# Kernel tuning notes

Measured on AMD Instinct MI355X. Metric: run time of the kernel, lower is better.

The kernel has to match this reference:

```python
import jax, jax.numpy as jnp
import numpy as np
import math

S, B, D_MODEL = 1024, 2, 1024
N_HEADS = 16
D_HEAD = D_MODEL // N_HEADS
C = 32  # compressed_len


def _xavier(key, shape):
    fan_in, fan_out = shape[-1], shape[-2] if len(shape) > 1 else shape[-1]
    limit = math.sqrt(6.0 / (fan_in + fan_out))
    return jax.random.uniform(key, shape, jnp.float32, -limit, limit)


def setup_inputs() -> dict:
    key = jax.random.key(0)
    ks = jax.random.split(key, 10)
    return {
        "x": jax.random.normal(ks[0], (S, B, D_MODEL), jnp.float32),
        "q_down": _xavier(ks[1], (C, D_MODEL)),
        "Wq": _xavier(ks[2], (D_MODEL, D_MODEL)),
        "bq": jnp.zeros((D_MODEL,), jnp.float32),
        "Wk": _xavier(ks[3], (D_MODEL, D_MODEL)),
        "bk": jnp.zeros((D_MODEL,), jnp.float32),
        "Wv": _xavier(ks[4], (D_MODEL, D_MODEL)),
        "bv": jnp.zeros((D_MODEL,), jnp.float32),
        "Wo": _xavier(ks[5], (D_MODEL, D_MODEL)),
        "bo": jnp.zeros((D_MODEL,), jnp.float32),
    }


def reference(x, q_down, Wq, bq, Wk, bk, Wv, bv, Wo, bo):
    # x: (s, b, d_model); causal=True, rope=None, dropout inactive (eval)
    s, b, d_model = x.shape
    h, dh = N_HEADS, D_HEAD
    scale = 1.0 / math.sqrt(dh)

    q_u = x @ Wq.T + bq                       # (s,b,dm)
    k_d = x @ Wk.T + bk
    v_d = x @ Wv.T + bv
    v_d_k = v_d @ Wk.T + bk
    v_d_v = v_d @ Wv.T + bv

    def heads(t):  # (s,b,dm) -> (b,h,s,dh)
        return t.reshape(s, b, h, dh).transpose(1, 2, 0, 3)

    q_u = heads(q_u) * scale
    k_d = heads(k_d)
    v_d_kv = jnp.concatenate([heads(v_d_k), heads(v_d_v)], axis=-1)  # (b,h,s,2dh)

    q_d = q_down.reshape(C, h, dh).transpose(1, 0, 2) * scale        # (h,c,dh)

    down = jnp.einsum('hcd,bhsd->bhcs', q_d, k_d)                    # (b,h,c,s)
    w = jnp.exp(down - jnp.max(down, axis=-1, keepdims=True))
    norm = jnp.cumsum(w, axis=-1)

    # (b,h,c,s,2dh): running compressed KV state
    kv_u = jnp.cumsum(w[..., None] * v_d_kv[:, :, None, :, :], axis=3) / norm[..., None]
    k_u, v_u = jnp.split(kv_u, 2, axis=-1)                           # each (b,h,c,s,dh)

    up = jnp.einsum('bhsd,bhcsd->bhsc', q_u, k_u)
    up = jax.nn.softmax(up, axis=-1)
    out = jnp.einsum('bhsc,bhcsd->bhsd', up, v_u)                    # (b,h,s,dh)

    out = out.transpose(2, 0, 1, 3).reshape(s, b, d_model)
    return out @ Wo.T + bo
```

## Files before the change

### kernel.cpp

```cpp
#include <hip/hip_runtime.h>
#include <cstdint>
#include <cstddef>

#define S_LEN 1024
#define BATCH 2
#define DM    1024
#define NH    16
#define DH    64
#define CC    32
#define SB    2048
#define TSD   128
#define NCHD  8

using short8 = __attribute__((ext_vector_type(8))) short;
using f32x4  = __attribute__((ext_vector_type(4))) float;

__device__ __forceinline__ float b2f(unsigned short u) {
    union { unsigned int i; float f; } v; v.i = ((unsigned int)u) << 16; return v.f;
}
__device__ __forceinline__ unsigned short f2b(float f) {
    union { float f; unsigned int i; } v; v.f = f;
    unsigned int x = v.i;
    unsigned int r = x + 0x7FFFu + ((x >> 16) & 1u);
    return (unsigned short)(r >> 16);
}

__device__ __forceinline__ void async_ld16(const unsigned short* g, unsigned short* l) {
    __builtin_amdgcn_global_load_lds(
        (const __attribute__((address_space(1))) unsigned int*)g,
        (__attribute__((address_space(3))) unsigned int*)l,
        16, 0, 0);
}

__global__ __launch_bounds__(256) void k_convert(
    const void* x, const void* qd,
    const void* wq, const void* wk, const void* wv, const void* wo,
    const void* bq, const void* bk, const void* bv, const void* bo,
    int* __restrict__ flag,
    unsigned short* xb, unsigned short* qdb,
    unsigned short* Wqb, unsigned short* Wkb, unsigned short* Wvb, unsigned short* Wob,
    float* biasf)
{
    __shared__ int cnt;
    if (threadIdx.x == 0) cnt = 0;
    __syncthreads();
    {
        const unsigned short* xs = (const unsigned short*)x;
        int local = 0;
        for (int i = threadIdx.x; i < 1024; i += 256) {
            unsigned e = (xs[i * 2] >> 7) & 0xFF;
            if (e >= 90 && e <= 160) local++;
        }
        atomicAdd(&cnt, local);
    }
    __syncthreads();
    const int isbf = (cnt >= 640);
    if (blockIdx.x == 0 && threadIdx.x == 0) *flag = isbf;

    const size_t tid = (size_t)blockIdx.x * 256 + threadIdx.x;
    const size_t stride = (size_t)gridDim.x * 256;

    auto cv = [&](const void* src, unsigned short* dst, size_t n) {
        if (isbf) {
            const short8* s = (const short8*)src;
            short8* d = (short8*)dst;
            for (size_t i = tid; i < n / 8; i += stride) d[i] = s[i];
        } else {
            const float4* s = (const float4*)src;
            for (size_t i = tid; i < n / 4; i += stride) {
                float4 v = s[i];
                ushort4 o;
                o.x = f2b(v.x); o.y = f2b(v.y); o.z = f2b(v.z); o.w = f2b(v.w);
                ((ushort4*)dst)[i] = o;
            }
        }
    };
    cv(x,  xb,  (size_t)SB * DM);
    cv(qd, qdb, (size_t)CC * DM);
    cv(wq, Wqb, (size_t)DM * DM);
    cv(wk, Wkb, (size_t)DM * DM);
    cv(wv, Wvb, (size_t)DM * DM);
    cv(wo, Wob, (size_t)DM * DM);
    for (size_t i = tid; i < 5 * DM; i += stride) {
        int w = (int)(i >> 10), o = (int)(i & 1023);
        float val;
        if (w == 4) val = 0.f;
        else {
            const void* bp = (w == 0) ? bq : ((w == 1) ? bk : ((w == 2) ? bv : bo));
            val = isbf ? b2f(((const unsigned short*)bp)[o]) : ((const float*)bp)[o];
        }
        biasf[i] = val;
    }
}

__global__ __launch_bounds__(256) void k_prep(const unsigned short* __restrict__ Wvb,
                                              const unsigned short* __restrict__ Wkb,
                                              const float* __restrict__ biasf,
                                              unsigned short* __restrict__ WvT,
                                              float* __restrict__ b2k,
                                              float* __restrict__ b2v)
{
    const int t = threadIdx.x;
    if (blockIdx.x < 128) {
        const int r0 = (blockIdx.x & 7) * 128;
        const int c0 = (blockIdx.x >> 3) * 64;
        __shared__ unsigned short T[128 * 68];
        for (int u = t; u < 128 * 8; u += 256) {
            int r = u >> 3, cb = (u & 7) * 8;
            *(short8*)&T[r * 68 + cb] = *(const short8*)&Wvb[(size_t)(r0 + r) * DM + c0 + cb];
        }
        __syncthreads();
        for (int u = t; u < 64 * 16; u += 256) {
            int c = u >> 4, r8 = (u & 15) * 8;
            short8 o;
#pragma unroll
            for (int k = 0; k < 8; ++k) o[k] = T[(r8 + k) * 68 + c];
            *(short8*)&WvT[(size_t)(c0 + c) * DM + r0 + r8] = o;
        }
    } else {
        const int idx = blockIdx.x - 128;
        const int set = idx >> 5;
        const int bx = idx & 31;
        const unsigned short* W = set ? Wvb : Wkb;
        const float* bvf = biasf + 2048;
        const float* badd = set ? (biasf + 2048) : (biasf + 1024);
        float* out = set ? b2v : b2k;
        const int w = t >> 6, l = t & 63;
        const int gw = bx * 4 + w;
        for (int i = 0; i < 8; ++i) {
            int row = gw * 8 + i;
            const unsigned short* wr = &W[(size_t)row * DM + l * 16];
            short8 a = *(const short8*)wr;
            short8 b = *(const short8*)(wr + 8);
            float s = 0.f;
#pragma unroll
            for (int j = 0; j < 8; ++j) {
                s += b2f((unsigned short)a[j]) * bvf[l * 16 + j];
                s += b2f((unsigned short)b[j]) * bvf[l * 16 + 8 + j];
            }
#pragma unroll
            for (int m = 1; m < 64; m <<= 1) s += __shfl_xor(s, m);
            if (l == 0) out[row] = s + badd[row];
        }
    }
}

struct GArg {
    const unsigned short* A;
    const unsigned short* Bt;
    const float* bias;
    void* out;
    float scale;
    int mode;
};

__device__ __forceinline__ int out_is_f32(int mode, const int* flag) {
    if (mode == 0) return 1;
    if (mode == 1) return 0;
    return (*flag == 0);
}

__global__ __launch_bounds__(256) void gemm_bt(GArg g0, GArg g1, GArg g2, GArg g3,
                                               const int* __restrict__ flag,
                                               int M, int N, int K)
{
    GArg ga = (blockIdx.z == 0) ? g0 : (blockIdx.z == 1) ? g1 : (blockIdx.z == 2) ? g2 : g3;
    const int m0 = blockIdx.y * 128;
    const int n0 = blockIdx.x * 128;
    __shared__ __align__(16) unsigned short As[2][128 * 32];
    __shared__ __align__(16) unsigned short Bs[2][128 * 32];
    const int t = threadIdx.x;
    const int w = t >> 6, l = t & 63;
    const int wy = w >> 1, wx = w & 1;
    const int lr = l >> 2;
    const int lk = (l & 3) * 8;
    const int ln = l & 15;
    const int lq = l >> 4;

    f32x4 acc[4][4] = {};

    const unsigned short* Ab0 = ga.A  + (size_t)(m0 + w * 32 +      lr) * K + lk;
    const unsigned short* Ab1 = ga.A  + (size_t)(m0 + w * 32 + 16 + lr) * K + lk;
    const unsigned short* Bb0 = ga.Bt + (size_t)(n0 + w * 32 +      lr) * K + lk;
    const unsigned short* Bb1 = ga.Bt + (size_t)(n0 + w * 32 + 16 + lr) * K + lk;

    for (int kk = 0; kk < K; kk += 64) {
#pragma unroll
        for (int hh = 0; hh < 2; ++hh) {
            async_ld16(Ab0 + kk + hh * 32, &As[hh][w * 1024]);
            async_ld16(Ab1 + kk + hh * 32, &As[hh][w * 1024 + 512]);
            async_ld16(Bb0 + kk + hh * 32, &Bs[hh][w * 1024]);
            async_ld16(Bb1 + kk + hh * 32, &Bs[hh][w * 1024 + 512]);
        }
        __syncthreads();
#pragma unroll
        for (int hh = 0; hh < 2; ++hh) {
            short8 af[4], bfr[4];
#pragma unroll
            for (int i = 0; i < 4; ++i)
                af[i] = *(const short8*)&As[hh][(wy * 64 + i * 16 + ln) * 32 + lq * 8];
#pragma unroll
            for (int j = 0; j < 4; ++j)
                bfr[j] = *(const short8*)&Bs[hh][(wx * 64 + j * 16 + ln) * 32 + lq * 8];
#pragma unroll
            for (int i = 0; i < 4; ++i)
#pragma unroll
                for (int j = 0; j < 4; ++j)
                    acc[i][j] = __builtin_amdgcn_mfma_f32_16x16x32_bf16(af[i], bfr[j], acc[i][j], 0, 0, 0);
        }
        __syncthreads();
    }

    const int f32o = out_is_f32(ga.mode, flag);
    const float sc = ga.scale;
#pragma unroll
    for (int j = 0; j < 4; ++j) {
        int col = n0 + wx * 64 + j * 16 + ln;
        float bv = ga.bias[col];
#pragma unroll
        for (int i = 0; i < 4; ++i) {
            int row0 = m0 + wy * 64 + i * 16 + lq * 4;
#pragma unroll
            for (int r = 0; r < 4; ++r) {
                float v = (acc[i][j][r] + bv) * sc;
                size_t idx = (size_t)(row0 + r) * N + col;
                if (f32o) ((float*)ga.out)[idx] = v;
                else      ((unsigned short*)ga.out)[idx] = f2b(v);
            }
        }
    }
}

__global__ __launch_bounds__(256) void gemm_bt_n64(GArg g0, GArg g1,
                                                   const int* __restrict__ flag,
                                                   int M, int N, int K)
{
    GArg ga = (blockIdx.z == 0) ? g0 : g1;
    const int m0 = blockIdx.y * 128;
    const int n0 = blockIdx.x * 64;
    __shared__ __align__(16) unsigned short As[2][128 * 32];
    __shared__ __align__(16) unsigned short Bs[2][64 * 32];
    const int t = threadIdx.x;
    const int w = t >> 6, l = t & 63;
    const int wy = w >> 1, wx = w & 1;
    const int lr = l >> 2;
    const int lk = (l & 3) * 8;
    const int ln = l & 15;
    const int lq = l >> 4;

    f32x4 acc[4][2] = {};

    const unsigned short* Ab0 = ga.A  + (size_t)(m0 + w * 32 +      lr) * K + lk;
    const unsigned short* Ab1 = ga.A  + (size_t)(m0 + w * 32 + 16 + lr) * K + lk;
    const unsigned short* Bb  = ga.Bt + (size_t)(n0 + w * 16 + lr) * K + lk;

    for (int kk = 0; kk < K; kk += 64) {
#pragma unroll
        for (int hh = 0; hh < 2; ++hh) {
            async_ld16(Ab0 + kk + hh * 32, &As[hh][w * 1024]);
            async_ld16(Ab1 + kk + hh * 32, &As[hh][w * 1024 + 512]);
            async_ld16(Bb  + kk + hh * 32, &Bs[hh][w * 512]);
        }
        __syncthreads();
#pragma unroll
        for (int hh = 0; hh < 2; ++hh) {
            short8 af[4], bfr[2];
#pragma unroll
            for (int i = 0; i < 4; ++i)
                af[i] = *(const short8*)&As[hh][(wy * 64 + i * 16 + ln) * 32 + lq * 8];
#pragma unroll
            for (int j = 0; j < 2; ++j)
                bfr[j] = *(const short8*)&Bs[hh][(wx * 32 + j * 16 + ln) * 32 + lq * 8];
#pragma unroll
            for (int i = 0; i < 4; ++i)
#pragma unroll
                for (int j = 0; j < 2; ++j)
                    acc[i][j] = __builtin_amdgcn_mfma_f32_16x16x32_bf16(af[i], bfr[j], acc[i][j], 0, 0, 0);
        }
        __syncthreads();
    }

    const int f32o = out_is_f32(ga.mode, flag);
    const float sc = ga.scale;
#pragma unroll
    for (int j = 0; j < 2; ++j) {
        int col = n0 + wx * 32 + j * 16 + ln;
        float bv = ga.bias[col];
#pragma unroll
        for (int i = 0; i < 4; ++i) {
            int row0 = m0 + wy * 64 + i * 16 + lq * 4;
#pragma unroll
            for (int r = 0; r < 4; ++r) {
                float v = (acc[i][j][r] + bv) * sc;
                size_t idx = (size_t)(row0 + r) * N + col;
                if (f32o) ((float*)ga.out)[idx] = v;
                else      ((unsigned short*)ga.out)[idx] = f2b(v);
            }
        }
    }
}

__global__ __launch_bounds__(256) void k_down(const unsigned short* __restrict__ kd,
                                              const unsigned short* __restrict__ qdw,
                                              float* __restrict__ wbuf,
                                              float* __restrict__ cmax,
                                              float* __restrict__ csum)
{
    const int bh = blockIdx.x;
    const int b = bh >> 4, h = bh & 15;
    const int chunk = blockIdx.y;
    const int s0 = chunk * TSD;
    const int t = threadIdx.x;

    __shared__ float qd[CC * DH];
    __shared__ float kt[TSD * DH];
    __shared__ float pm[CC * 8];
    __shared__ float cmf[CC];

    for (int idx = t; idx < CC * DH; idx += 256)
        qd[idx] = b2f(qdw[(idx >> 6) * DM + h * DH + (idx & 63)]);
    for (int u = t; u < TSD * DH / 8; u += 256) {
        int sl = u >> 3, d8 = (u & 7) * 8;
        short8 v = *(const short8*)&kd[(size_t)((s0 + sl) * BATCH + b) * DM + h * DH + d8];
#pragma unroll
        for (int j = 0; j < 8; ++j) kt[sl * DH + d8 + j] = b2f((unsigned short)v[j]);
    }
    __syncthreads();

    const int c = t & 31;
    float s16[16];
    float lmax = -3.4e38f;
    int it = 0;
    for (int idx = t; idx < CC * TSD; idx += 256, ++it) {
        int sl = idx >> 5;
        float s = 0.f;
#pragma unroll
        for (int d = 0; d < DH; d += 4) {
            float4 qa = *(const float4*)&qd[c * DH + d];
            float4 kb = *(const float4*)&kt[sl * DH + d];
            s += qa.x * kb.x + qa.y * kb.y + qa.z * kb.z + qa.w * kb.w;
        }
        s *= 0.125f;
        wbuf[((size_t)bh * CC + c) * S_LEN + s0 + sl] = s;
        s16[it] = s;
        lmax = fmaxf(lmax, s);
    }
    pm[c * 8 + (t >> 5)] = lmax;
    __syncthreads();
    if (t < CC) {
        float m = pm[t * 8];
#pragma unroll
        for (int g = 1; g < 8; ++g) m = fmaxf(m, pm[t * 8 + g]);
        cmf[t] = m;
        cmax[((size_t)bh * CC + t) * NCHD + chunk] = m;
    }
    __syncthreads();
    const float cm = cmf[c];
    float es = 0.f;
#pragma unroll
    for (int k = 0; k < 16; ++k) es += __expf(s16[k] - cm);
    pm[c * 8 + (t >> 5)] = es;
    __syncthreads();
    if (t < CC) {
        float ssum = pm[t * 8];
#pragma unroll
        for (int g = 1; g < 8; ++g) ssum += pm[t * 8 + g];
        csum[((size_t)bh * CC + t) * NCHD + chunk] = ssum;
    }
}

__global__ __launch_bounds__(256) void k_wapply(const float* __restrict__ wbuf,
                                                const float* __restrict__ cmax,
                                                const float* __restrict__ csum,
                                                unsigned short* __restrict__ wb,
                                                unsigned short* __restrict__ wT,
                                                float* __restrict__ invn)
{
    const int bh = blockIdx.x, seg = blockIdx.y;
    const int t = threadIdx.x;
    __shared__ float gm[CC];
    __shared__ float basep[CC];
    __shared__ float psum[CC][9];
    __shared__ unsigned short wTt[128 * 40];
    __shared__ float invt[128 * 36];

    if (t < CC) {
        const size_t cb = (size_t)(bh * CC + t) * NCHD;
        float m = cmax[cb];
#pragma unroll
        for (int g = 1; g < NCHD; ++g) m = fmaxf(m, cmax[cb + g]);
        gm[t] = m;
        float bsum = 0.f;
        for (int k = 0; k < seg; ++k)
            bsum += csum[cb + k] * __expf(cmax[cb + k] - m);
        basep[t] = bsum;
    }
    __syncthreads();

    const int c = t >> 3, sub = t & 7;
    const float gmc = gm[c];
    const size_t rbase = (size_t)bh * 32768 + c * 1024 + seg * 128 + sub * 16;
    float w16[16];
    float s = 0.f;
#pragma unroll
    for (int i = 0; i < 16; ++i) {
        float v = __expf(wbuf[rbase + i] - gmc);
        w16[i] = v; s += v;
    }
    psum[c][sub] = s;
    short8 o0, o1;
#pragma unroll
    for (int i = 0; i < 8; ++i) { o0[i] = f2b(w16[i]); o1[i] = f2b(w16[8 + i]); }
    *(short8*)&wb[rbase] = o0;
    *(short8*)&wb[rbase + 8] = o1;
#pragma unroll
    for (int i = 0; i < 16; ++i) wTt[(sub * 16 + i) * 40 + c] = f2b(w16[i]);
    __syncthreads();

    float run = basep[c];
    for (int k = 0; k < sub; ++k) run += psum[c][k];
#pragma unroll
    for (int i = 0; i < 16; ++i) {
        run += w16[i];
        invt[(sub * 16 + i) * 36 + c] = 1.0f / fmaxf(run, 1e-30f);
    }
    __syncthreads();

    for (int u = t; u < 128 * 4; u += 256) {
        int r = u >> 2, cb = (u & 3) * 8;
        *(short8*)&wT[(size_t)bh * 32768 + (seg * 128 + r) * 32 + cb] =
            *(const short8*)&wTt[r * 40 + cb];
    }
    for (int u = t; u < 128 * 8; u += 256) {
        int r = u >> 3, cb = (u & 7) * 4;
        *(float4*)&invn[(size_t)bh * 32768 + (seg * 128 + r) * 32 + cb] =
            *(const float4*)&invt[r * 36 + cb];
    }
}

__global__ __launch_bounds__(256) void k_state(const unsigned short* __restrict__ wb,
                                               const unsigned short* __restrict__ vdk,
                                               const unsigned short* __restrict__ vdv,
                                               float* __restrict__ Mst,
                                               float* __restrict__ NTst)
{
    const int bh = blockIdx.x, ch = blockIdx.y;
    const int b = bh >> 4, h = bh & 15;
    const int s0 = ch * 64;
    const int t = threadIdx.x;
    const int w = t >> 6, l = t & 63;
    const int ln = l & 15, lq = l >> 4;
    __shared__ __align__(16) unsigned short Ws[32 * 72];
    __shared__ __align__(16) unsigned short T1[64 * 72];
    __shared__ __align__(16) unsigned short T2[64 * 72];
    __shared__ __align__(16) unsigned short KT[64 * 72];
    __shared__ __align__(16) unsigned short VT[64 * 72];

    for (int u = t; u < 32 * 8; u += 256) {
        int r = u >> 3, cb = (u & 7) * 8;
        *(short8*)&Ws[r * 72 + cb] = *(const short8*)&wb[(size_t)bh * 32768 + r * 1024 + s0 + cb];
    }
    for (int u = t; u < 64 * 8; u += 256) {
        int r = u >> 3, cb = (u & 7) * 8;
        *(short8*)&T1[r * 72 + cb] =
            *(const short8*)&vdk[(size_t)((s0 + r) * BATCH + b) * DM + h * DH + cb];
        *(short8*)&T2[r * 72 + cb] =
            *(const short8*)&vdv[(size_t)((s0 + r) * BATCH + b) * DM + h * DH + cb];
    }
    __syncthreads();
    for (int u = t; u < 64 * 8; u += 256) {
        int d = u >> 3, s8 = (u & 7) * 8;
        short8 o1, o2;
#pragma unroll
        for (int k = 0; k < 8; ++k) {
            o1[k] = T1[(s8 + k) * 72 + d];
            o2[k] = T2[(s8 + k) * 72 + d];
        }
        *(short8*)&KT[d * 72 + s8] = o1;
        *(short8*)&VT[d * 72 + s8] = o2;
    }
    __syncthreads();

    f32x4 accM[2] = {};
#pragma unroll
    for (int ks = 0; ks < 2; ++ks) {
        short8 b8 = *(const short8*)&KT[(w * 16 + ln) * 72 + ks * 32 + lq * 8];
#pragma unroll
        for (int i = 0; i < 2; ++i) {
            short8 a8 = *(const short8*)&Ws[(i * 16 + ln) * 72 + ks * 32 + lq * 8];
            accM[i] = __builtin_amdgcn_mfma_f32_16x16x32_bf16(a8, b8, accM[i], 0, 0, 0);
        }
    }
#pragma unroll
    for (int i = 0; i < 2; ++i)
#pragma unroll
        for (int r = 0; r < 4; ++r)
            Mst[((size_t)(bh * 16 + ch) * 32 + i * 16 + lq * 4 + r) * 64 + w * 16 + ln] = accM[i][r];

    f32x4 accN[2] = {};
#pragma unroll
    for (int ks = 0; ks < 2; ++ks) {
        short8 a8 = *(const short8*)&VT[(w * 16 + ln) * 72 + ks * 32 + lq * 8];
#pragma unroll
        for (int j = 0; j < 2; ++j) {
            short8 b8 = *(const short8*)&Ws[(j * 16 + ln) * 72 + ks * 32 + lq * 8];
            accN[j] = __builtin_amdgcn_mfma_f32_16x16x32_bf16(a8, b8, accN[j], 0, 0, 0);
        }
    }
#pragma unroll
    for (int j = 0; j < 2; ++j)
#pragma unroll
        for (int r = 0; r < 4; ++r)
            NTst[((size_t)(bh * 16 + ch) * 64 + w * 16 + lq * 4 + r) * 32 + j * 16 + ln] = accN[j][r];
}

__global__ __launch_bounds__(256) void k_prefix(const float* __restrict__ Mst,
                                                const float* __restrict__ NTst,
                                                unsigned short* __restrict__ Mcum,
                                                unsigned short* __restrict__ NTcum)
{
    const int bh = blockIdx.x;
    const float* src = blockIdx.y ? NTst : Mst;
    unsigned short* dst = blockIdx.y ? NTcum : Mcum;
    const int e0 = threadIdx.x * 8;
    float run[8];
#pragma unroll
    for (int j = 0; j < 8; ++j) run[j] = 0.f;
    for (int ch = 0; ch < 16; ++ch) {
        size_t off = (size_t)(bh * 16 + ch) * 2048 + e0;
        short8 ob;
#pragma unroll
        for (int j = 0; j < 8; ++j) ob[j] = f2b(run[j]);
        *(short8*)&dst[off] = ob;
#pragma unroll
        for (int j = 0; j < 8; ++j) run[j] += src[off + j];
    }
}

__global__ __launch_bounds__(256) void k_att(
    const unsigned short* __restrict__ qu,
    const unsigned short* __restrict__ vdk,
    const unsigned short* __restrict__ wb,
    const float* __restrict__ invn,
    const unsigned short* __restrict__ wT,
    const unsigned short* __restrict__ vdv,
    const unsigned short* __restrict__ Mcum,
    const unsigned short* __restrict__ NTcum,
    unsigned short* __restrict__ attout)
{
    const int bh = blockIdx.x, b = bh >> 4, h = bh & 15;
    const int qi = blockIdx.y;
    const int s0 = qi * 64;
    const int t = threadIdx.x;
    const int w = t >> 6, l = t & 63;
    const int wy = w >> 1, wx = w & 1;
    const int ln = l & 15, lq = l >> 4;

    __shared__ __align__(16) unsigned short Qs[64 * 72];
    __shared__ __align__(16) unsigned short Gs[64 * 72];
    __shared__ __align__(16) unsigned short Kd[64 * 72];
    __shared__ __align__(16) unsigned short Wd[32 * 72];
    __shared__ __align__(16) unsigned short WTd[64 * 40];
    __shared__ __align__(16) unsigned short VTd[64 * 72];
    __shared__ __align__(16) unsigned short Mc[32 * 72];
    __shared__ __align__(16) unsigned short Nc[64 * 40];

    for (int u = t; u < 64 * 8; u += 256) {
        int r = u >> 3, cb = (u & 7) * 8;
        *(short8*)&Qs[r * 72 + cb] =
            *(const short8*)&qu[(size_t)(s0 + r) * 2048 + b * 1024 + h * 64 + cb];
        *(short8*)&Kd[r * 72 + cb] =
            *(const short8*)&vdk[(size_t)(s0 + r) * 2048 + b * 1024 + h * 64 + cb];
        *(short8*)&Gs[r * 72 + cb] =
            *(const short8*)&vdv[(size_t)(s0 + r) * 2048 + b * 1024 + h * 64 + cb];
    }
    for (int u = t; u < 32 * 8; u += 256) {
        int r = u >> 3, cb = (u & 7) * 8;
        *(short8*)&Wd[r * 72 + cb] =
            *(const short8*)&wb[(size_t)bh * 32768 + r * 1024 + s0 + cb];
        *(short8*)&Mc[r * 72 + cb] =
            *(const short8*)&Mcum[((size_t)(bh * 16 + qi) * 32 + r) * 64 + cb];
    }
    for (int u = t; u < 64 * 4; u += 256) {
        int r = u >> 2, cb = (u & 3) * 8;
        *(short8*)&WTd[r * 40 + cb] =
            *(const short8*)&wT[(size_t)bh * 32768 + (s0 + r) * 32 + cb];
        *(short8*)&Nc[r * 40 + cb] =
            *(const short8*)&NTcum[((size_t)(bh * 16 + qi) * 64 + r) * 32 + cb];
    }
    __syncthreads();

    for (int u = t; u < 64 * 8; u += 256) {
        int d = u >> 3, s8 = (u & 7) * 8;
        short8 o;
#pragma unroll
        for (int k = 0; k < 8; ++k) o[k] = Gs[(s8 + k) * 72 + d];
        *(short8*)&VTd[d * 72 + s8] = o;
    }
    __syncthreads();

    {
        f32x4 accG[2][2] = {};
#pragma unroll
        for (int ks = 0; ks < 2; ++ks) {
            short8 a8[2], b8[2];
#pragma unroll
            for (int i = 0; i < 2; ++i)
                a8[i] = *(const short8*)&Qs[(wy * 32 + i * 16 + ln) * 72 + ks * 32 + lq * 8];
#pragma unroll
            for (int j = 0; j < 2; ++j)
                b8[j] = *(const short8*)&Kd[(wx * 32 + j * 16 + ln) * 72 + ks * 32 + lq * 8];
#pragma unroll
            for (int i = 0; i < 2; ++i)
#pragma unroll
                for (int j = 0; j < 2; ++j)
                    accG[i][j] = __builtin_amdgcn_mfma_f32_16x16x32_bf16(a8[i], b8[j], accG[i][j], 0, 0, 0);
        }
        __syncthreads();
#pragma unroll
        for (int i = 0; i < 2; ++i) {
            int row = wy * 32 + i * 16 + lq * 4;
#pragma unroll
            for (int j = 0; j < 2; ++j) {
                int col = wx * 32 + j * 16 + ln;
#pragma unroll
                for (int r = 0; r < 4; ++r) {
                    float v = accG[i][j][r];
                    if (col > row + r) v = 0.f;
                    Gs[(row + r) * 72 + col] = f2b(v);
                }
            }
        }
    }
    __syncthreads();

    f32x4 accU[2] = {};
#pragma unroll
    for (int ks = 0; ks < 2; ++ks) {
        short8 ga = *(const short8*)&Gs[(w * 16 + ln) * 72 + ks * 32 + lq * 8];
        short8 qa = *(const short8*)&Qs[(w * 16 + ln) * 72 + ks * 32 + lq * 8];
#pragma unroll
        for (int j = 0; j < 2; ++j) {
            short8 wf = *(const short8*)&Wd[(j * 16 + ln) * 72 + ks * 32 + lq * 8];
            short8 mf = *(const short8*)&Mc[(j * 16 + ln) * 72 + ks * 32 + lq * 8];
            accU[j] = __builtin_amdgcn_mfma_f32_16x16x32_bf16(ga, wf, accU[j], 0, 0, 0);
            accU[j] = __builtin_amdgcn_mfma_f32_16x16x32_bf16(qa, mf, accU[j], 0, 0, 0);
        }
    }
    __syncthreads();

    {
        int rowl = w * 16 + lq * 4;
#pragma unroll
        for (int r = 0; r < 4; ++r) {
            int srow = s0 + rowl + r;
            float inv0 = invn[(size_t)bh * 32768 + srow * 32 + ln];
            float inv1 = invn[(size_t)bh * 32768 + srow * 32 + 16 + ln];
            float l0 = accU[0][r] * inv0;
            float l1 = accU[1][r] * inv1;
            float m = fmaxf(l0, l1);
#pragma unroll
            for (int msk = 1; msk < 16; msk <<= 1) m = fmaxf(m, __shfl_xor(m, msk));
            float e0 = __expf(l0 - m), e1 = __expf(l1 - m);
            float Z = e0 + e1;
#pragma unroll
            for (int msk = 1; msk < 16; msk <<= 1) Z += __shfl_xor(Z, msk);
            float iz = 1.0f / Z;
            Qs[(rowl + r) * 40 + ln]      = f2b(e0 * iz * inv0);
            Qs[(rowl + r) * 40 + 16 + ln] = f2b(e1 * iz * inv1);
        }
    }
    __syncthreads();

    short8 pa[2];
#pragma unroll
    for (int i = 0; i < 2; ++i)
        pa[i] = *(const short8*)&Qs[(wy * 32 + i * 16 + ln) * 40 + lq * 8];
    {
        f32x4 accS[2][2] = {};
        short8 b8[2];
#pragma unroll
        for (int j = 0; j < 2; ++j)
            b8[j] = *(const short8*)&WTd[(wx * 32 + j * 16 + ln) * 40 + lq * 8];
#pragma unroll
        for (int i = 0; i < 2; ++i)
#pragma unroll
            for (int j = 0; j < 2; ++j)
                accS[i][j] = __builtin_amdgcn_mfma_f32_16x16x32_bf16(pa[i], b8[j], accS[i][j], 0, 0, 0);
#pragma unroll
        for (int i = 0; i < 2; ++i) {
            int row = wy * 32 + i * 16 + lq * 4;
#pragma unroll
            for (int j = 0; j < 2; ++j) {
                int col = wx * 32 + j * 16 + ln;
#pragma unroll
                for (int r = 0; r < 4; ++r) {
                    float v = accS[i][j][r];
                    if (col > row + r) v = 0.f;
                    Gs[(row + r) * 72 + col] = f2b(v);
                }
            }
        }
    }
    __syncthreads();

    {
        f32x4 accO[2][2] = {};
        short8 n8[2];
#pragma unroll
        for (int j = 0; j < 2; ++j)
            n8[j] = *(const short8*)&Nc[(wx * 32 + j * 16 + ln) * 40 + lq * 8];
#pragma unroll
        for (int i = 0; i < 2; ++i)
#pragma unroll
            for (int j = 0; j < 2; ++j)
                accO[i][j] = __builtin_amdgcn_mfma_f32_16x16x32_bf16(pa[i], n8[j], accO[i][j], 0, 0, 0);
#pragma unroll
        for (int ks = 0; ks < 2; ++ks) {
            short8 a8[2], b8[2];
#pragma unroll
            for (int i = 0; i < 2; ++i)
                a8[i] = *(const short8*)&Gs[(wy * 32 + i * 16 + ln) * 72 + ks * 32 + lq * 8];
#pragma unroll
            for (int j = 0; j < 2; ++j)
                b8[j] = *(const short8*)&VTd[(wx * 32 + j * 16 + ln) * 72 + ks * 32 + lq * 8];
#pragma unroll
            for (int i = 0; i < 2; ++i)
#pragma unroll
                for (int j = 0; j < 2; ++j)
                    accO[i][j] = __builtin_amdgcn_mfma_f32_16x16x32_bf16(a8[i], b8[j], accO[i][j], 0, 0, 0);
        }
#pragma unroll
        for (int i = 0; i < 2; ++i) {
            int rowb = s0 + wy * 32 + i * 16 + lq * 4;
#pragma unroll
            for (int j = 0; j < 2; ++j) {
                int d = wx * 32 + j * 16 + ln;
#pragma unroll
                for (int r = 0; r < 4; ++r)
                    attout[(size_t)(rowb + r) * 2048 + b * 1024 + h * 64 + d] = f2b(accO[i][j][r]);
            }
        }
    }
}

extern "C" void kernel_launch(void* const* d_in, const int* in_sizes, int n_in,
                              void* d_out, int out_size, void* d_ws, size_t ws_size,
                              hipStream_t stream)
{
    (void)in_sizes; (void)n_in; (void)out_size; (void)ws_size;
    char* ws = (char*)d_ws;
    const size_t MB = (size_t)1 << 20;
    const size_t KB = (size_t)1 << 10;
    unsigned short* attout = (unsigned short*)(ws + 0 * MB);
    unsigned short* q_u    = (unsigned short*)(ws + 4 * MB);
    unsigned short* k_d    = (unsigned short*)(ws + 8 * MB);
    unsigned short* v_dk   = (unsigned short*)(ws + 12 * MB);
    unsigned short* v_dv   = (unsigned short*)(ws + 16 * MB);
    float* wbuf = (float*)(ws + 20 * MB);
    unsigned short* wb  = (unsigned short*)(ws + 24 * MB);
    unsigned short* wT  = (unsigned short*)(ws + 26 * MB);
    float* invn = (float*)(ws + 28 * MB);
    float* Mst  = (float*)(ws + 32 * MB);
    float* NTst = (float*)(ws + 36 * MB);
    unsigned short* Mcum  = (unsigned short*)(ws + 40 * MB);
    unsigned short* NTcum = (unsigned short*)(ws + 42 * MB);
    unsigned short* xb  = (unsigned short*)(ws + 44 * MB);
    unsigned short* Wqb = (unsigned short*)(ws + 48 * MB);
    unsigned short* Wkb = (unsigned short*)(ws + 50 * MB);
    unsigned short* Wvb = (unsigned short*)(ws + 52 * MB);
    unsigned short* Wob = (unsigned short*)(ws + 54 * MB);
    unsigned short* WvT = (unsigned short*)(ws + 56 * MB);
    unsigned short* W2k = (unsigned short*)(ws + 58 * MB);
    unsigned short* W2v = (unsigned short*)(ws + 60 * MB);
    unsigned short* qdb = (unsigned short*)(ws + 62 * MB);
    float* biasf  = (float*)(ws + 62 * MB + 64 * KB);
    float* b2k    = (float*)(ws + 62 * MB + 128 * KB);
    float* b2v    = (float*)(ws + 62 * MB + 132 * KB);
    float* cmax   = (float*)(ws + 62 * MB + 192 * KB);
    float* csum   = (float*)(ws + 62 * MB + 256 * KB);
    int*   flag   = (int*)  (ws + 62 * MB + 320 * KB);

    k_convert<<<1024, 256, 0, stream>>>(
        d_in[0], d_in[1], d_in[2], d_in[4], d_in[6], d_in[8],
        d_in[3], d_in[5], d_in[7], d_in[9],
        flag, xb, qdb, Wqb, Wkb, Wvb, Wob, biasf);

    const float* bqf = biasf;
    const float* bkf = biasf + 1024;
    const float* bof = biasf + 3072;
    const float* zerof = biasf + 4096;

    k_prep<<<192, 256, 0, stream>>>(Wvb, Wkb, biasf, WvT, b2k, b2v);
    GArg wpk{ Wkb, WvT, zerof, (void*)W2k, 1.0f, 1 };
    GArg wpv{ Wvb, WvT, zerof, (void*)W2v, 1.0f, 1 };
    gemm_bt_n64<<<dim3(16, 8, 2), 256, 0, stream>>>(wpk, wpv, flag, DM, DM, DM);

    GArg gq { xb, Wqb, bqf, (void*)q_u, 0.125f, 1 };
    GArg gk { xb, Wkb, bkf, (void*)k_d, 1.0f, 1 };
    GArg gvk{ xb, W2k, b2k, (void*)v_dk, 1.0f, 1 };
    GArg gvv{ xb, W2v, b2v, (void*)v_dv, 1.0f, 1 };
    gemm_bt<<<dim3(8, 16, 4), 256, 0, stream>>>(gq, gk, gvk, gvv, flag, SB, DM, DM);

    k_down<<<dim3(32, NCHD), 256, 0, stream>>>(k_d, qdb, wbuf, cmax, csum);
    k_wapply<<<dim3(32, 8), 256, 0, stream>>>(wbuf, cmax, csum, wb, wT, invn);
    k_state<<<dim3(32, 16), 256, 0, stream>>>(wb, v_dk, v_dv, Mst, NTst);
    k_prefix<<<dim3(32, 2), 256, 0, stream>>>(Mst, NTst, Mcum, NTcum);
    k_att<<<dim3(32, 16), 256, 0, stream>>>(q_u, v_dk, wb, invn, wT, v_dv, Mcum, NTcum, attout);

    GArg go{ attout, Wob, bof, d_out, 1.0f, 2 };
    gemm_bt_n64<<<dim3(16, 16, 1), 256, 0, stream>>>(go, go, flag, SB, DM, DM);
}
```

Before: 197.8 us.

## Skip bf16 input copies by reading raw inputs directly; use MFMA in k_down

When the inputs are detected as bf16, the convert kernel no longer copies x and the weights into workspace buffers. Downstream kernels instead pick the raw input pointers at runtime from the flag. Separately, k_down's fp32 scalar dot products for the compressed-query scores are replaced with bf16 MFMA, and the max/sum reductions move to shuffles over a shared score tile. With fp32 inputs (the test case) the first change does nothing except add a flag read per kernel, while the MFMA path runs unconditionally.

Measured after the change: 188.9 us. 4.5% less time.

```diff
diff --git a/kernel.cpp b/kernel.cpp
--- a/kernel.cpp
+++ b/kernel.cpp
@@ -60,12 +60,8 @@
     const size_t tid = (size_t)blockIdx.x * 256 + threadIdx.x;
     const size_t stride = (size_t)gridDim.x * 256;
 
-    auto cv = [&](const void* src, unsigned short* dst, size_t n) {
-        if (isbf) {
-            const short8* s = (const short8*)src;
-            short8* d = (short8*)dst;
-            for (size_t i = tid; i < n / 8; i += stride) d[i] = s[i];
-        } else {
+    if (!isbf) {
+        auto cv = [&](const void* src, unsigned short* dst, size_t n) {
             const float4* s = (const float4*)src;
             for (size_t i = tid; i < n / 4; i += stride) {
                 float4 v = s[i];
@@ -73,14 +69,14 @@
                 o.x = f2b(v.x); o.y = f2b(v.y); o.z = f2b(v.z); o.w = f2b(v.w);
                 ((ushort4*)dst)[i] = o;
             }
-        }
-    };
-    cv(x,  xb,  (size_t)SB * DM);
-    cv(qd, qdb, (size_t)CC * DM);
-    cv(wq, Wqb, (size_t)DM * DM);
-    cv(wk, Wkb, (size_t)DM * DM);
-    cv(wv, Wvb, (size_t)DM * DM);
-    cv(wo, Wob, (size_t)DM * DM);
+        };
+        cv(x,  xb,  (size_t)SB * DM);
+        cv(qd, qdb, (size_t)CC * DM);
+        cv(wq, Wqb, (size_t)DM * DM);
+        cv(wk, Wkb, (size_t)DM * DM);
+        cv(wv, Wvb, (size_t)DM * DM);
+        cv(wo, Wob, (size_t)DM * DM);
+    }
     for (size_t i = tid; i < 5 * DM; i += stride) {
         int w = (int)(i >> 10), o = (int)(i & 1023);
         float val;
@@ -93,13 +89,19 @@
     }
 }
 
-__global__ __launch_bounds__(256) void k_prep(const unsigned short* __restrict__ Wvb,
-                                              const unsigned short* __restrict__ Wkb,
+__global__ __launch_bounds__(256) void k_prep(const unsigned short* __restrict__ Wv0,
+                                              const unsigned short* __restrict__ Wv1,
+                                              const unsigned short* __restrict__ Wk0,
+                                              const unsigned short* __restrict__ Wk1,
+                                              const int* __restrict__ flag,
                                               const float* __restrict__ biasf,
                                               unsigned short* __restrict__ WvT,
                                               float* __restrict__ b2k,
                                               float* __restrict__ b2v)
 {
+    const int isbf = *flag;
+    const unsigned short* Wvb = isbf ? Wv1 : Wv0;
+    const unsigned short* Wkb = isbf ? Wk1 : Wk0;
     const int t = threadIdx.x;
     if (blockIdx.x < 128) {
         const int r0 = (blockIdx.x & 7) * 128;
@@ -146,25 +148,24 @@
 }
 
 struct GArg {
-    const unsigned short* A;
-    const unsigned short* Bt;
+    const unsigned short* A0;
+    const unsigned short* A1;
+    const unsigned short* B0;
+    const unsigned short* B1;
     const float* bias;
     void* out;
     float scale;
     int mode;
 };
 
-__device__ __forceinline__ int out_is_f32(int mode, const int* flag) {
-    if (mode == 0) return 1;
-    if (mode == 1) return 0;
-    return (*flag == 0);
-}
-
 __global__ __launch_bounds__(256) void gemm_bt(GArg g0, GArg g1, GArg g2, GArg g3,
                                                const int* __restrict__ flag,
                                                int M, int N, int K)
 {
     GArg ga = (blockIdx.z == 0) ? g0 : (blockIdx.z == 1) ? g1 : (blockIdx.z == 2) ? g2 : g3;
+    const int isbf = *flag;
+    const unsigned short* Ap = isbf ? ga.A1 : ga.A0;
+    const unsigned short* Bp = isbf ? ga.B1 : ga.B0;
     const int m0 = blockIdx.y * 128;
     const int n0 = blockIdx.x * 128;
     __shared__ __align__(16) unsigned short As[2][128 * 32];
@@ -179,10 +180,10 @@
 
     f32x4 acc[4][4] = {};
 
-    const unsigned short* Ab0 = ga.A  + (size_t)(m0 + w * 32 +      lr) * K + lk;
-    const unsigned short* Ab1 = ga.A  + (size_t)(m0 + w * 32 + 16 + lr) * K + lk;
-    const unsigned short* Bb0 = ga.Bt + (size_t)(n0 + w * 32 +      lr) * K + lk;
-    const unsigned short* Bb1 = ga.Bt + (size_t)(n0 + w * 32 + 16 + lr) * K + lk;
+    const unsigned short* Ab0 = Ap + (size_t)(m0 + w * 32 +      lr) * K + lk;
+    const unsigned short* Ab1 = Ap + (size_t)(m0 + w * 32 + 16 + lr) * K + lk;
+    const unsigned short* Bb0 = Bp + (size_t)(n0 + w * 32 +      lr) * K + lk;
+    const unsigned short* Bb1 = Bp + (size_t)(n0 + w * 32 + 16 + lr) * K + lk;
 
     for (int kk = 0; kk < K; kk += 64) {
 #pragma unroll
@@ -211,7 +212,7 @@
         __syncthreads();
     }
 
-    const int f32o = out_is_f32(ga.mode, flag);
+    const int f32o = (ga.mode == 0) ? 1 : (ga.mode == 1) ? 0 : (!isbf);
     const float sc = ga.scale;
 #pragma unroll
     for (int j = 0; j < 4; ++j) {
@@ -236,6 +237,9 @@
                                                    int M, int N, int K)
 {
     GArg ga = (blockIdx.z == 0) ? g0 : g1;
+    const int isbf = *flag;
+    const unsigned short* Ap = isbf ? ga.A1 : ga.A0;
+    const unsigned short* Bp = isbf ? ga.B1 : ga.B0;
     const int m0 = blockIdx.y * 128;
     const int n0 = blockIdx.x * 64;
     __shared__ __align__(16) unsigned short As[2][128 * 32];
@@ -250,9 +254,9 @@
 
     f32x4 acc[4][2] = {};
 
-    const unsigned short* Ab0 = ga.A  + (size_t)(m0 + w * 32 +      lr) * K + lk;
-    const unsigned short* Ab1 = ga.A  + (size_t)(m0 + w * 32 + 16 + lr) * K + lk;
-    const unsigned short* Bb  = ga.Bt + (size_t)(n0 + w * 16 + lr) * K + lk;
+    const unsigned short* Ab0 = Ap + (size_t)(m0 + w * 32 +      lr) * K + lk;
+    const unsigned short* Ab1 = Ap + (size_t)(m0 + w * 32 + 16 + lr) * K + lk;
+    const unsigned short* Bb  = Bp + (size_t)(n0 + w * 16 + lr) * K + lk;
 
     for (int kk = 0; kk < K; kk += 64) {
 #pragma unroll
@@ -280,7 +284,7 @@
         __syncthreads();
     }
 
-    const int f32o = out_is_f32(ga.mode, flag);
+    const int f32o = (ga.mode == 0) ? 1 : (ga.mode == 1) ? 0 : (!isbf);
     const float sc = ga.scale;
 #pragma unroll
     for (int j = 0; j < 2; ++j) {
@@ -301,72 +305,91 @@
 }
 
 __global__ __launch_bounds__(256) void k_down(const unsigned short* __restrict__ kd,
-                                              const unsigned short* __restrict__ qdw,
+                                              const unsigned short* __restrict__ qd0,
+                                              const unsigned short* __restrict__ qd1,
+                                              const int* __restrict__ flag,
                                               float* __restrict__ wbuf,
                                               float* __restrict__ cmax,
                                               float* __restrict__ csum)
 {
+    const unsigned short* qdw = (*flag) ? qd1 : qd0;
     const int bh = blockIdx.x;
     const int b = bh >> 4, h = bh & 15;
     const int chunk = blockIdx.y;
     const int s0 = chunk * TSD;
     const int t = threadIdx.x;
-
-    __shared__ float qd[CC * DH];
-    __shared__ float kt[TSD * DH];
-    __shared__ float pm[CC * 8];
+    const int w = t >> 6, l = t & 63;
+    const int ln = l & 15, lq = l >> 4;
+
+    __shared__ __align__(16) unsigned short QD[32 * 72];
+    __shared__ __align__(16) unsigned short KT[128 * 72];
+    __shared__ float SS[32 * 132];
+    __shared__ float pm[256];
     __shared__ float cmf[CC];
 
-    for (int idx = t; idx < CC * DH; idx += 256)
-        qd[idx] = b2f(qdw[(idx >> 6) * DM + h * DH + (idx & 63)]);
-    for (int u = t; u < TSD * DH / 8; u += 256) {
-        int sl = u >> 3, d8 = (u & 7) * 8;
-        short8 v = *(const short8*)&kd[(size_t)((s0 + sl) * BATCH + b) * DM + h * DH + d8];
-#pragma unroll
-        for (int j = 0; j < 8; ++j) kt[sl * DH + d8 + j] = b2f((unsigned short)v[j]);
-    }
-    __syncthreads();
-
-    const int c = t & 31;
-    float s16[16];
+    {
+        int r = t >> 3, cb = (t & 7) * 8;
+        *(short8*)&QD[r * 72 + cb] = *(const short8*)&qdw[(size_t)r * DM + h * DH + cb];
+    }
+    for (int u = t; u < 128 * 8; u += 256) {
+        int r = u >> 3, cb = (u & 7) * 8;
+        *(short8*)&KT[r * 72 + cb] =
+            *(const short8*)&kd[(size_t)((s0 + r) * BATCH + b) * DM + h * DH + cb];
+    }
+    __syncthreads();
+
+    f32x4 accG[2][2] = {};
+#pragma unroll
+    for (int ks = 0; ks < 2; ++ks) {
+        short8 a8[2], b8[2];
+#pragma unroll
+        for (int i = 0; i < 2; ++i)
+            a8[i] = *(const short8*)&QD[(i * 16 + ln) * 72 + ks * 32 + lq * 8];
+#pragma unroll
+        for (int j = 0; j < 2; ++j)
+            b8[j] = *(const short8*)&KT[(w * 32 + j * 16 + ln) * 72 + ks * 32 + lq * 8];
+#pragma unroll
+        for (int i = 0; i < 2; ++i)
+#pragma unroll
+            for (int j = 0; j < 2; ++j)
+                accG[i][j] = __builtin_amdgcn_mfma_f32_16x16x32_bf16(a8[i], b8[j], accG[i][j], 0, 0, 0);
+    }
+#pragma unroll
+    for (int i = 0; i < 2; ++i) {
+#pragma unroll
+        for (int j = 0; j < 2; ++j) {
+            int sl = w * 32 + j * 16 + ln;
+#pragma unroll
+            for (int r = 0; r < 4; ++r) {
+                int c = i * 16 + lq * 4 + r;
+                float v = accG[i][j][r] * 0.125f;
+                SS[c * 132 + sl] = v;
+                wbuf[((size_t)bh * CC + c) * S_LEN + s0 + sl] = v;
+            }
+        }
+    }
+    __syncthreads();
+
+    const int c = t >> 3, sub = t & 7;
     float lmax = -3.4e38f;
-    int it = 0;
-    for (int idx = t; idx < CC * TSD; idx += 256, ++it) {
-        int sl = idx >> 5;
-        float s = 0.f;
-#pragma unroll
-        for (int d = 0; d < DH; d += 4) {
-            float4 qa = *(const float4*)&qd[c * DH + d];
-            float4 kb = *(const float4*)&kt[sl * DH + d];
-            s += qa.x * kb.x + qa.y * kb.y + qa.z * kb.z + qa.w * kb.w;
-        }
-        s *= 0.125f;
-        wbuf[((size_t)bh * CC + c) * S_LEN + s0 + sl] = s;
-        s16[it] = s;
-        lmax = fmaxf(lmax, s);
-    }
-    pm[c * 8 + (t >> 5)] = lmax;
-    __syncthreads();
-    if (t < CC) {
-        float m = pm[t * 8];
-#pragma unroll
-        for (int g = 1; g < 8; ++g) m = fmaxf(m, pm[t * 8 + g]);
-        cmf[t] = m;
-        cmax[((size_t)bh * CC + t) * NCHD + chunk] = m;
+#pragma unroll
+    for (int k = 0; k < 16; ++k) lmax = fmaxf(lmax, SS[c * 132 + sub * 16 + k]);
+    lmax = fmaxf(lmax, __shfl_xor(lmax, 1));
+    lmax = fmaxf(lmax, __shfl_xor(lmax, 2));
+    lmax = fmaxf(lmax, __shfl_xor(lmax, 4));
+    if (sub == 0) {
+        cmf[c] = lmax;
+        cmax[((size_t)bh * CC + c) * NCHD + chunk] = lmax;
     }
     __syncthreads();
     const float cm = cmf[c];
     float es = 0.f;
 #pragma unroll
-    for (int k = 0; k < 16; ++k) es += __expf(s16[k] - cm);
-    pm[c * 8 + (t >> 5)] = es;
-    __syncthreads();
-    if (t < CC) {
-        float ssum = pm[t * 8];
-#pragma unroll
-        for (int g = 1; g < 8; ++g) ssum += pm[t * 8 + g];
-        csum[((size_t)bh * CC + t) * NCHD + chunk] = ssum;
-    }
+    for (int k = 0; k < 16; ++k) es += __expf(SS[c * 132 + sub * 16 + k] - cm);
+    es += __shfl_xor(es, 1);
+    es += __shfl_xor(es, 2);
+    es += __shfl_xor(es, 4);
+    if (sub == 0) csum[((size_t)bh * CC + c) * NCHD + chunk] = es;
 }
 
 __global__ __launch_bounds__(256) void k_wapply(const float* __restrict__ wbuf,
@@ -781,6 +804,13 @@
     float* csum   = (float*)(ws + 62 * MB + 256 * KB);
     int*   flag   = (int*)  (ws + 62 * MB + 320 * KB);
 
+    const unsigned short* xraw  = (const unsigned short*)d_in[0];
+    const unsigned short* qdraw = (const unsigned short*)d_in[1];
+    const unsigned short* wqraw = (const unsigned short*)d_in[2];
+    const unsigned short* wkraw = (const unsigned short*)d_in[4];
+    const unsigned short* wvraw = (const unsigned short*)d_in[6];
+    const unsigned short* woraw = (const unsigned short*)d_in[8];
+
     k_convert<<<1024, 256, 0, stream>>>(
         d_in[0], d_in[1], d_in[2], d_in[4], d_in[6], d_in[8],
         d_in[3], d_in[5], d_in[7], d_in[9],
@@ -791,23 +821,23 @@
     const float* bof = biasf + 3072;
     const float* zerof = biasf + 4096;
 
-    k_prep<<<192, 256, 0, stream>>>(Wvb, Wkb, biasf, WvT, b2k, b2v);
-    GArg wpk{ Wkb, WvT, zerof, (void*)W2k, 1.0f, 1 };
-    GArg wpv{ Wvb, WvT, zerof, (void*)W2v, 1.0f, 1 };
+    k_prep<<<192, 256, 0, stream>>>(Wvb, wvraw, Wkb, wkraw, flag, biasf, WvT, b2k, b2v);
+    GArg wpk{ Wkb, wkraw, WvT, WvT, zerof, (void*)W2k, 1.0f, 1 };
+    GArg wpv{ Wvb, wvraw, WvT, WvT, zerof, (void*)W2v, 1.0f, 1 };
     gemm_bt_n64<<<dim3(16, 8, 2), 256, 0, stream>>>(wpk, wpv, flag, DM, DM, DM);
 
-    GArg gq { xb, Wqb, bqf, (void*)q_u, 0.125f, 1 };
-    GArg gk { xb, Wkb, bkf, (void*)k_d, 1.0f, 1 };
-    GArg gvk{ xb, W2k, b2k, (void*)v_dk, 1.0f, 1 };
-    GArg gvv{ xb, W2v, b2v, (void*)v_dv, 1.0f, 1 };
+    GArg gq { xb, xraw, Wqb, wqraw, bqf, (void*)q_u, 0.125f, 1 };
+    GArg gk { xb, xraw, Wkb, wkraw, bkf, (void*)k_d, 1.0f, 1 };
+    GArg gvk{ xb, xraw, W2k, W2k,   b2k, (void*)v_dk, 1.0f, 1 };
+    GArg gvv{ xb, xraw, W2v, W2v,   b2v, (void*)v_dv, 1.0f, 1 };
     gemm_bt<<<dim3(8, 16, 4), 256, 0, stream>>>(gq, gk, gvk, gvv, flag, SB, DM, DM);
 
-    k_down<<<dim3(32, NCHD), 256, 0, stream>>>(k_d, qdb, wbuf, cmax, csum);
+    k_down<<<dim3(32, NCHD), 256, 0, stream>>>(k_d, qdb, qdraw, flag, wbuf, cmax, csum);
     k_wapply<<<dim3(32, 8), 256, 0, stream>>>(wbuf, cmax, csum, wb, wT, invn);
     k_state<<<dim3(32, 16), 256, 0, stream>>>(wb, v_dk, v_dv, Mst, NTst);
     k_prefix<<<dim3(32, 2), 256, 0, stream>>>(Mst, NTst, Mcum, NTcum);
     k_att<<<dim3(32, 16), 256, 0, stream>>>(q_u, v_dk, wb, invn, wT, v_dv, Mcum, NTcum, attout);
 
-    GArg go{ attout, Wob, bof, d_out, 1.0f, 2 };
+    GArg go{ attout, attout, Wob, woraw, bof, d_out, 1.0f, 2 };
     gemm_bt_n64<<<dim3(16, 16, 1), 256, 0, stream>>>(go, go, flag, SB, DM, DM);
 }
```
